# Optimization experiments

Measured on AMD Instinct MI355X. Metric: run time of the kernel, lower is better.

## Reference

```python
import jax, jax.numpy as jnp
import numpy as np

N_GRAMS = 3
N_KERNELS = 11

def _kernel_mus(K):
    l = [1.0]
    if K == 1:
        return l
    bs = 2.0 / (K - 1)
    l.append(1.0 - bs / 2.0)
    for i in range(1, K - 1):
        l.append(l[i] - bs)
    return l

def _kernel_sigmas(K):
    if K == 1:
        return [0.001]
    bs = 2.0 / (K - 1)
    return [0.001] + [0.5 * bs] * (K - 1)

MU = jnp.asarray(_kernel_mus(N_KERNELS), jnp.float32)       # (K,)
SIGMA = jnp.asarray(_kernel_sigmas(N_KERNELS), jnp.float32)  # (K,)

def _conv_relu(x, w, b):
    # x: (B,E,L), w: (O,E,h); right-pad h-1 so output length == L (as ConstantPad1d((0,h-1)))
    h = w.shape[-1]
    y = jax.lax.conv_general_dilated(x, w, (1,), [(0, h - 1)], dimension_numbers=('NCH', 'OIH', 'NCH'))
    return jax.nn.relu(y + b[None, :, None]).transpose(0, 2, 1)  # (B,L,O)

def _cosine(a, b):
    # CosineMatrixAttention: normalize rows then matmul
    an = a / (jnp.linalg.norm(a, axis=-1, keepdims=True) + 1e-13)
    bn = b / (jnp.linalg.norm(b, axis=-1, keepdims=True) + 1e-13)
    return jnp.einsum('bqe,bde->bqd', an, bn)

def setup_inputs() -> dict:
    key = jax.random.key(0)
    ks = jax.random.split(key, 12)
    B, Lq, Ld, V, E, O = 128, 64, 512, 30000, 300, 128
    inp = {}
    inp['tokens_q'] = jax.random.randint(ks[0], (B, Lq), 0, V)
    inp['tokens_d'] = jax.random.randint(ks[1], (B, Ld), 0, V)
    inp['emb'] = jax.random.normal(ks[2], (V, E), jnp.float32) * 0.1
    for i, h in enumerate((1, 2, 3)):
        inp['conv_w%d' % h] = jax.random.normal(ks[3 + i], (O, E, h), jnp.float32) * (1.0 / np.sqrt(E * h))
        inp['conv_b%d' % h] = jnp.zeros((O,), jnp.float32)
    inp['fc_w'] = jax.random.normal(ks[9], (1, N_KERNELS * N_GRAMS * N_GRAMS), jnp.float32) * 0.1
    inp['fc_b'] = jnp.zeros((1,), jnp.float32)
    return inp

def reference(tokens_q, tokens_d, emb, conv_w1, conv_b1, conv_w2, conv_b2, conv_w3, conv_b3, fc_w, fc_b):
    qmask = (tokens_q > 0).astype(jnp.float32)  # (B,Lq)
    dmask = (tokens_d > 0).astype(jnp.float32)  # (B,Ld)
    qe = emb[tokens_q].transpose(0, 2, 1)  # (B,E,Lq)
    de = emb[tokens_d].transpose(0, 2, 1)  # (B,E,Ld)
    cws = [(conv_w1, conv_b1), (conv_w2, conv_b2), (conv_w3, conv_b3)]
    hq = [_conv_relu(qe, w, b) for w, b in cws]  # each (B,Lq,O)
    hd = [_conv_relu(de, w, b) for w, b in cws]  # each (B,Ld,O)
    pair_mask = qmask[:, :, None] * dmask[:, None, :]  # (B,Lq,Ld)
    mu = MU[None, None, None, :]
    sig = SIGMA[None, None, None, :]
    feats = []
    for q in range(N_GRAMS):
        for d in range(N_GRAMS):
            m = _cosine(hq[q], hd[d]) * pair_mask  # (B,Lq,Ld)
            rbf = jnp.exp(-jnp.square(m[..., None] - mu) / (2.0 * jnp.square(sig))) * pair_mask[..., None]
            qk = rbf.sum(axis=2)  # (B,Lq,K)
            logk = jnp.log(jnp.maximum(qk, 1e-10)) * 0.01
            # NOTE: original has a typo (loq_ vs log_) so the query mask is NOT applied before summing
            feats.append(logk.sum(axis=1))  # (B,K)
    cross = jnp.concatenate(feats, axis=-1)  # (B, K*G*G)
    return cross @ fc_w.T + fc_b  # (B,1)
```

## Files before the change

kernel.cpp:

```cpp
#include <hip/hip_runtime.h>
#include <hip/hip_bf16.h>

typedef __attribute__((ext_vector_type(8))) short short8;
typedef __attribute__((ext_vector_type(4))) float f32x4;
typedef __attribute__((ext_vector_type(2))) unsigned int u32x2;

#define E_DIM 300
#define NCH   128
#define NOUT  384
#define NCHUNK 30

#define OPITCH 792

#define GLD16(gp, lp) __builtin_amdgcn_global_load_lds( \
    (const __attribute__((address_space(1))) unsigned int*)(const void*)(gp), \
    (__attribute__((address_space(3))) unsigned int*)(void*)(lp), 16, 0, 0)

__device__ __forceinline__ unsigned short f2bf(float f) {
    unsigned int u = __float_as_uint(f);
    u += 0x7FFFu + ((u >> 16) & 1u);
    return (unsigned short)(u >> 16);
}

__device__ __forceinline__ void xcd_map(int bx, int& b, int& p) {
    int x = bx & 7;
    int j = bx >> 3;
    b = x * 16 + j / 9;
    p = j - (j / 9) * 9;
}

__global__ void pack_wb(const float* __restrict__ w1, const float* __restrict__ w2,
                        const float* __restrict__ w3, unsigned short* __restrict__ Wp) {
    int idx = blockIdx.x * 256 + threadIdx.x;
    if (idx >= NCHUNK * NOUT * 32) return;
    int ke = idx & 31;
    int n  = (idx >> 5) % NOUT;
    int c  = idx / (32 * NOUT);
    int s  = c / 10;
    int e  = (c % 10) * 32 + ke;
    int g  = n >> 7, o = n & 127, h = g + 1;
    float v = 0.0f;
    if (e < E_DIM && s < h) {
        const float* w = (g == 0) ? w1 : ((g == 1) ? w2 : w3);
        v = w[(o * E_DIM + e) * h + s];
    }
    Wp[idx] = f2bf(v);
}

__global__ void pack_emb(const float* __restrict__ emb, unsigned short* __restrict__ embh) {
    int u = blockIdx.x * 256 + threadIdx.x;
    if (u >= 30000 * 40) return;
    int row = u / 40;
    int c8  = u - row * 40;
    int col = c8 * 8;
    ushort4 lo = {0, 0, 0, 0}, hi = {0, 0, 0, 0};
    const float* src = emb + (size_t)row * E_DIM + col;
    if (col + 8 <= E_DIM) {
        float4 a = *(const float4*)src;
        float4 c = *(const float4*)(src + 4);
        lo.x = f2bf(a.x); lo.y = f2bf(a.y); lo.z = f2bf(a.z); lo.w = f2bf(a.w);
        hi.x = f2bf(c.x); hi.y = f2bf(c.y); hi.z = f2bf(c.z); hi.w = f2bf(c.w);
    } else if (col < E_DIM) {
        float4 a = *(const float4*)src;
        lo.x = f2bf(a.x); lo.y = f2bf(a.y); lo.z = f2bf(a.z); lo.w = f2bf(a.w);
    }
    unsigned short* dst = embh + (size_t)row * 320 + col;
    *(ushort4*)dst       = lo;
    *(ushort4*)(dst + 4) = hi;
}

__launch_bounds__(512, 4)
__global__ void conv_mfma(const int* __restrict__ tokens_q, const int* __restrict__ tokens_d,
                          const unsigned short* __restrict__ embh, const unsigned short* __restrict__ Wp,
                          const float* __restrict__ b1, const float* __restrict__ b2,
                          const float* __restrict__ b3,
                          unsigned short* __restrict__ hq, unsigned short* __restrict__ hd) {
    __shared__ __align__(16) char lds[64 * OPITCH];
    __shared__ float nrm[64 * 3];

    int b, tile;
    xcd_map(blockIdx.x, b, tile);
    int isq  = (tile == 0);
    int L    = isq ? 64 : 512;
    int t0   = isq ? 0 : (tile - 1) * 64;
    const int* toks = isq ? (tokens_q + b * 64) : (tokens_d + b * 512);
    int tid  = threadIdx.x;
    int lane = tid & 63;
    int wn   = tid >> 6;
    int lr   = lane & 15;
    int lg   = lane >> 4;

    if (tid < 192) nrm[tid] = 0.0f;

    const unsigned short* __restrict__ wpB = Wp + (size_t)(wn * 16 + lr) * 32 + lg * 8;
    short8 bb[2][3];
    #pragma unroll
    for (int g = 0; g < 3; ++g) {
        bb[0][g] = *(const short8*)(wpB + (size_t)(0 * NOUT + g * 128) * 32);
        bb[1][g] = *(const short8*)(wpB + (size_t)(1 * NOUT + g * 128) * 32);
    }

    {
        auto gather_row = [&](int r, int sl) {
            int pos = t0 + r;
            int tk  = (pos < L) ? toks[pos] : -1;
            char* wbase = lds + r * 640;
            int xr = (r & 7) << 4;
            if (tk >= 0) {
                const unsigned short* src = embh + (size_t)tk * 320 + sl * 8;
                uint4 v[5];
                #pragma unroll
                for (int k = 0; k < 5; ++k) v[k] = *(const uint4*)(src + k * 64);
                #pragma unroll
                for (int k = 0; k < 5; ++k)
                    *(uint4*)(wbase + (((sl + 8 * k) * 16) ^ xr)) = v[k];
            } else {
                uint4 z = {0, 0, 0, 0};
                #pragma unroll
                for (int k = 0; k < 5; ++k)
                    *(uint4*)(wbase + (((sl + 8 * k) * 16) ^ xr)) = z;
            }
        };
        gather_row(tid >> 3, tid & 7);
        if (tid < 16) gather_row(64 + (tid >> 3), tid & 7);
    }
    __syncthreads();

    f32x4 acc[4][3];
    #pragma unroll
    for (int i = 0; i < 4; ++i)
        #pragma unroll
        for (int g = 0; g < 3; ++g) acc[i][g] = (f32x4){0.f, 0.f, 0.f, 0.f};

    #pragma unroll
    for (int c = 0; c < NCHUNK; ++c) {
        const int S  = (c >= 20) ? 2 : ((c >= 10) ? 1 : 0);
        const int ec = c - S * 10;
        short8 a[4];
        #pragma unroll
        for (int i = 0; i < 4; ++i) {
            int row = i * 16 + lr + S;
            int byt = (ec * 64 + lg * 16) ^ ((row & 7) << 4);
            a[i] = *(const short8*)(lds + row * 640 + byt);
        }
        #pragma unroll
        for (int i = 0; i < 4; ++i)
            #pragma unroll
            for (int g = S; g < 3; ++g)
                acc[i][g] = __builtin_amdgcn_mfma_f32_16x16x32_bf16(a[i], bb[c & 1][g], acc[i][g], 0, 0, 0);
        if (c < NCHUNK - 2) {
            const int S2 = ((c + 2) >= 20) ? 2 : (((c + 2) >= 10) ? 1 : 0);
            #pragma unroll
            for (int g = S2; g < 3; ++g)
                bb[c & 1][g] = *(const short8*)(wpB + (size_t)((c + 2) * NOUT + g * 128) * 32);
        }
    }

    #pragma unroll
    for (int g = 0; g < 3; ++g) {
        float bv = (g == 0 ? b1 : (g == 1 ? b2 : b3))[wn * 16 + lr];
        #pragma unroll
        for (int i = 0; i < 4; ++i)
            #pragma unroll
            for (int r = 0; r < 4; ++r) {
                float v = acc[i][g][r] + bv;
                v = v > 0.0f ? v : 0.0f;
                acc[i][g][r] = v;
                float s = v * v;
                s += __shfl_xor(s, 1, 16);
                s += __shfl_xor(s, 2, 16);
                s += __shfl_xor(s, 4, 16);
                s += __shfl_xor(s, 8, 16);
                if (lr == 0) atomicAdd(&nrm[(i * 16 + lg * 4 + r) * 3 + g], s);
            }
    }
    __syncthreads();

    if (tid < 192) nrm[tid] = 1.0f / (sqrtf(nrm[tid]) + 1e-13f);
    __syncthreads();

    unsigned short* os = (unsigned short*)lds;
    #pragma unroll
    for (int i = 0; i < 4; ++i)
        #pragma unroll
        for (int r = 0; r < 4; ++r) {
            int row = i * 16 + lg * 4 + r;
            #pragma unroll
            for (int g = 0; g < 3; ++g)
                os[row * (OPITCH / 2) + g * 128 + wn * 16 + lr] = f2bf(acc[i][g][r] * nrm[row * 3 + g]);
        }
    __syncthreads();

    unsigned short* outp = isq ? hq : hd;
    #pragma unroll
    for (int it = 0; it < 12; ++it) {
        int idx = it * 512 + tid;
        int row = idx / 96;
        int c8  = idx - row * 96;
        int g   = c8 >> 5;
        int ch  = (c8 & 31) * 4;
        u32x2 v = *(const u32x2*)(lds + row * OPITCH + c8 * 8);
        __builtin_nontemporal_store(v, (u32x2*)&outp[((size_t)(g * 128 + b) * L + t0 + row) * NCH + ch]);
    }
}

__launch_bounds__(256, 2)
__global__ void sim_rbf(const unsigned short* __restrict__ hq,
                        const unsigned short* __restrict__ hd,
                        const int* __restrict__ tokens_q, const int* __restrict__ tokens_d,
                        float* __restrict__ cross) {
    __shared__ __align__(16) short ds2[2][64 * 128];
    __shared__ unsigned char dm_s[512];
    __shared__ float logk_s[11];

    int b, p;
    xcd_map(blockIdx.x, b, p);
    int gq = p / 3;
    int gd = p % 3;
    int tid = threadIdx.x;
    int lane = tid & 63;
    int wn   = tid >> 6;
    int lr   = lane & 15;
    int lg   = lane >> 4;

    if (tid < 11) logk_s[tid] = 0.0f;

    const unsigned short* qsrc = hq + ((size_t)(gq * 128 + b) * 64) * NCH;
    const unsigned short* dsrc = hd + ((size_t)(gd * 128 + b) * 512) * NCH;

    int q  = wn * 16 + lr;
    float qm = (tokens_q[b * 64 + q] > 0) ? 1.0f : 0.0f;

    int rloc = 4 * wn + (lane >> 4);
    int cu   = (lane & 15) ^ (rloc & 7);

    auto stage = [&](int bufI, int ch) {
        const unsigned short* s0 = dsrc + ((size_t)ch * 64 + rloc) * NCH + cu * 8;
        #pragma unroll
        for (int it = 0; it < 4; ++it)
            GLD16(s0 + (size_t)it * 16 * NCH, &ds2[bufI][(it * 16 + 4 * wn) * 128]);
    };

    stage(0, 0);
    for (int i = tid; i < 512; i += 256)
        dm_s[i] = (tokens_d[b * 512 + i] > 0) ? 1 : 0;
    __syncthreads();

    float qk[11];
    #pragma unroll
    for (int k = 0; k < 11; ++k) qk[k] = 0.0f;

    const float C4 = 0.0183156389f;

    for (int ch = 0; ch < 8; ++ch) {
        int buf = ch & 1;
        if (ch < 7) stage(buf ^ 1, ch + 1);

        short8 qf[4];
        #pragma unroll
        for (int ks = 0; ks < 4; ++ks)
            qf[ks] = *(const short8*)&qsrc[q * NCH + ks * 32 + lg * 8];

        #pragma unroll
        for (int mt = 0; mt < 4; ++mt) {
            int r = mt * 16 + lr;
            f32x4 acc = (f32x4){0.f, 0.f, 0.f, 0.f};
            #pragma unroll
            for (int ks = 0; ks < 4; ++ks) {
                short8 a = *(const short8*)((const char*)&ds2[buf][0]
                              + r * 256 + (((ks * 4 + lg) ^ (r & 7)) << 4));
                acc = __builtin_amdgcn_mfma_f32_16x16x32_bf16(a, qf[ks], acc, 0, 0, 0);
            }
            uchar4 du = *(const uchar4*)&dm_s[ch * 64 + mt * 16 + lg * 4];
            float cv[4], cm[4];
            cm[0] = qm * (float)du.x; cm[1] = qm * (float)du.y;
            cm[2] = qm * (float)du.z; cm[3] = qm * (float)du.w;
            #pragma unroll
            for (int r2 = 0; r2 < 4; ++r2) cv[r2] = acc[r2] * cm[r2];

            float cmx = fmaxf(fmaxf(cv[0], cv[1]), fmaxf(cv[2], cv[3]));
            if (__any(cmx > 0.98f)) {
                #pragma unroll
                for (int r2 = 0; r2 < 4; ++r2) {
                    if (cv[r2] > 0.98f) {
                        float t0 = cv[r2] - 1.0f;
                        qk[0] += __expf(-500000.0f * t0 * t0);
                    }
                }
            }
            #pragma unroll
            for (int r2 = 0; r2 < 4; ++r2) {
                float c  = cv[r2];
                float tA = c - 0.1f;
                float TA = __expf(-50.0f * tA * tA) * cm[r2];
                float UA = __expf(20.0f * c - 4.0f);
                float s  = C4 * __builtin_amdgcn_rcpf(UA);
                float TB = TA * s;
                float UB = C4 * s;
                qk[5] += TA;
                TA *= UA; qk[4] += TA; UA *= C4;
                TA *= UA; qk[3] += TA; UA *= C4;
                TA *= UA; qk[2] += TA; UA *= C4;
                TA *= UA; qk[1] += TA;
                qk[6] += TB;
                TB *= UB; qk[7] += TB; UB *= C4;
                TB *= UB; qk[8] += TB; UB *= C4;
                TB *= UB; qk[9] += TB; UB *= C4;
                TB *= UB; qk[10] += TB;
            }
        }

        __syncthreads();
    }

    #pragma unroll
    for (int k = 0; k < 11; ++k) {
        float v = qk[k];
        v += __shfl_xor(v, 16);
        v += __shfl_xor(v, 32);
        qk[k] = v;
    }
    if (lg == 0) {
        #pragma unroll
        for (int k = 0; k < 11; ++k) {
            float lv = __logf(fmaxf(qk[k], 1e-10f)) * 0.01f;
            atomicAdd(&logk_s[k], lv);
        }
    }
    __syncthreads();
    if (tid < 11) cross[b * 99 + p * 11 + tid] = logk_s[tid];
}

__global__ void fc_kernel(const float* __restrict__ cross, const float* __restrict__ fc_w,
                          const float* __restrict__ fc_b, float* __restrict__ out) {
    int b = threadIdx.x;
    float acc = fc_b[0];
    #pragma unroll 11
    for (int j = 0; j < 99; ++j) acc += cross[b * 99 + j] * fc_w[j];
    out[b] = acc;
}

extern "C" void kernel_launch(void* const* d_in, const int* in_sizes, int n_in,
                              void* d_out, int out_size, void* d_ws, size_t ws_size,
                              hipStream_t stream) {
    const int*   tq  = (const int*)d_in[0];
    const int*   td  = (const int*)d_in[1];
    const float* emb = (const float*)d_in[2];
    const float* w1  = (const float*)d_in[3];
    const float* cb1 = (const float*)d_in[4];
    const float* w2  = (const float*)d_in[5];
    const float* cb2 = (const float*)d_in[6];
    const float* w3  = (const float*)d_in[7];
    const float* cb3 = (const float*)d_in[8];
    const float* fcw = (const float*)d_in[9];
    const float* fcb = (const float*)d_in[10];

    char* ws = (char*)d_ws;
    unsigned short* Wp    = (unsigned short*)ws;
    float*          cross = (float*)(ws + 921600);
    unsigned short* hq    = (unsigned short*)(ws + 1048576);
    unsigned short* hd    = (unsigned short*)(ws + 8388608);
    unsigned short* embh  = (unsigned short*)(ws + 58720256);

    hipLaunchKernelGGL(pack_wb, dim3(1440), dim3(256), 0, stream, w1, w2, w3, Wp);
    hipLaunchKernelGGL(pack_emb, dim3(4688), dim3(256), 0, stream, emb, embh);
    hipLaunchKernelGGL(conv_mfma, dim3(128 * 9), dim3(512), 0, stream,
                       tq, td, embh, Wp, cb1, cb2, cb3, hq, hd);
    hipLaunchKernelGGL(sim_rbf, dim3(128 * 9), dim3(256), 0, stream, hq, hd, tq, td, cross);
    hipLaunchKernelGGL(fc_kernel, dim3(1), dim3(128), 0, stream, cross, fcw, fcb, (float*)d_out);
}
```

Baseline: 171.3 us.

## Merge pack kernels and read doc tiles directly from global in sim_rbf

```diff
diff --git a/kernel.cpp b/kernel.cpp
--- a/kernel.cpp
+++ b/kernel.cpp
@@ -11,10 +11,6 @@
 #define NCHUNK 30
 
 #define OPITCH 792
-
-#define GLD16(gp, lp) __builtin_amdgcn_global_load_lds( \
-    (const __attribute__((address_space(1))) unsigned int*)(const void*)(gp), \
-    (__attribute__((address_space(3))) unsigned int*)(void*)(lp), 16, 0, 0)
 
 __device__ __forceinline__ unsigned short f2bf(float f) {
     unsigned int u = __float_as_uint(f);
@@ -29,44 +25,46 @@
     p = j - (j / 9) * 9;
 }
 
-__global__ void pack_wb(const float* __restrict__ w1, const float* __restrict__ w2,
-                        const float* __restrict__ w3, unsigned short* __restrict__ Wp) {
-    int idx = blockIdx.x * 256 + threadIdx.x;
-    if (idx >= NCHUNK * NOUT * 32) return;
-    int ke = idx & 31;
-    int n  = (idx >> 5) % NOUT;
-    int c  = idx / (32 * NOUT);
-    int s  = c / 10;
-    int e  = (c % 10) * 32 + ke;
-    int g  = n >> 7, o = n & 127, h = g + 1;
-    float v = 0.0f;
-    if (e < E_DIM && s < h) {
-        const float* w = (g == 0) ? w1 : ((g == 1) ? w2 : w3);
-        v = w[(o * E_DIM + e) * h + s];
-    }
-    Wp[idx] = f2bf(v);
-}
-
-__global__ void pack_emb(const float* __restrict__ emb, unsigned short* __restrict__ embh) {
-    int u = blockIdx.x * 256 + threadIdx.x;
-    if (u >= 30000 * 40) return;
-    int row = u / 40;
-    int c8  = u - row * 40;
-    int col = c8 * 8;
-    ushort4 lo = {0, 0, 0, 0}, hi = {0, 0, 0, 0};
-    const float* src = emb + (size_t)row * E_DIM + col;
-    if (col + 8 <= E_DIM) {
-        float4 a = *(const float4*)src;
-        float4 c = *(const float4*)(src + 4);
-        lo.x = f2bf(a.x); lo.y = f2bf(a.y); lo.z = f2bf(a.z); lo.w = f2bf(a.w);
-        hi.x = f2bf(c.x); hi.y = f2bf(c.y); hi.z = f2bf(c.z); hi.w = f2bf(c.w);
-    } else if (col < E_DIM) {
-        float4 a = *(const float4*)src;
-        lo.x = f2bf(a.x); lo.y = f2bf(a.y); lo.z = f2bf(a.z); lo.w = f2bf(a.w);
-    }
-    unsigned short* dst = embh + (size_t)row * 320 + col;
-    *(ushort4*)dst       = lo;
-    *(ushort4*)(dst + 4) = hi;
+__global__ void pack_all(const float* __restrict__ w1, const float* __restrict__ w2,
+                         const float* __restrict__ w3, const float* __restrict__ emb,
+                         unsigned short* __restrict__ Wp, unsigned short* __restrict__ embh) {
+    int bx = blockIdx.x;
+    if (bx < 1440) {
+        int idx = bx * 256 + threadIdx.x;
+        if (idx >= NCHUNK * NOUT * 32) return;
+        int ke = idx & 31;
+        int n  = (idx >> 5) % NOUT;
+        int c  = idx / (32 * NOUT);
+        int s  = c / 10;
+        int e  = (c % 10) * 32 + ke;
+        int g  = n >> 7, o = n & 127, h = g + 1;
+        float v = 0.0f;
+        if (e < E_DIM && s < h) {
+            const float* w = (g == 0) ? w1 : ((g == 1) ? w2 : w3);
+            v = w[(o * E_DIM + e) * h + s];
+        }
+        Wp[idx] = f2bf(v);
+    } else {
+        int u = (bx - 1440) * 256 + threadIdx.x;
+        if (u >= 30000 * 40) return;
+        int row = u / 40;
+        int c8  = u - row * 40;
+        int col = c8 * 8;
+        ushort4 lo = {0, 0, 0, 0}, hi = {0, 0, 0, 0};
+        const float* src = emb + (size_t)row * E_DIM + col;
+        if (col + 8 <= E_DIM) {
+            float4 a = *(const float4*)src;
+            float4 c = *(const float4*)(src + 4);
+            lo.x = f2bf(a.x); lo.y = f2bf(a.y); lo.z = f2bf(a.z); lo.w = f2bf(a.w);
+            hi.x = f2bf(c.x); hi.y = f2bf(c.y); hi.z = f2bf(c.z); hi.w = f2bf(c.w);
+        } else if (col < E_DIM) {
+            float4 a = *(const float4*)src;
+            lo.x = f2bf(a.x); lo.y = f2bf(a.y); lo.z = f2bf(a.z); lo.w = f2bf(a.w);
+        }
+        unsigned short* dst = embh + (size_t)row * 320 + col;
+        *(ushort4*)dst       = lo;
+        *(ushort4*)(dst + 4) = hi;
+    }
 }
 
 __launch_bounds__(512, 4)
@@ -209,7 +207,6 @@
                         const unsigned short* __restrict__ hd,
                         const int* __restrict__ tokens_q, const int* __restrict__ tokens_d,
                         float* __restrict__ cross) {
-    __shared__ __align__(16) short ds2[2][64 * 128];
     __shared__ unsigned char dm_s[512];
     __shared__ float logk_s[11];
 
@@ -224,6 +221,8 @@
     int lg   = lane >> 4;
 
     if (tid < 11) logk_s[tid] = 0.0f;
+    for (int i = tid; i < 512; i += 256)
+        dm_s[i] = (tokens_d[b * 512 + i] > 0) ? 1 : 0;
 
     const unsigned short* qsrc = hq + ((size_t)(gq * 128 + b) * 64) * NCH;
     const unsigned short* dsrc = hd + ((size_t)(gd * 128 + b) * 512) * NCH;
@@ -231,19 +230,11 @@
     int q  = wn * 16 + lr;
     float qm = (tokens_q[b * 64 + q] > 0) ? 1.0f : 0.0f;
 
-    int rloc = 4 * wn + (lane >> 4);
-    int cu   = (lane & 15) ^ (rloc & 7);
-
-    auto stage = [&](int bufI, int ch) {
-        const unsigned short* s0 = dsrc + ((size_t)ch * 64 + rloc) * NCH + cu * 8;
-        #pragma unroll
-        for (int it = 0; it < 4; ++it)
-            GLD16(s0 + (size_t)it * 16 * NCH, &ds2[bufI][(it * 16 + 4 * wn) * 128]);
-    };
-
-    stage(0, 0);
-    for (int i = tid; i < 512; i += 256)
-        dm_s[i] = (tokens_d[b * 512 + i] > 0) ? 1 : 0;
+    short8 qf[4];
+    #pragma unroll
+    for (int ks = 0; ks < 4; ++ks)
+        qf[ks] = *(const short8*)&qsrc[q * NCH + ks * 32 + lg * 8];
+
     __syncthreads();
 
     float qk[11];
@@ -253,22 +244,13 @@
     const float C4 = 0.0183156389f;
 
     for (int ch = 0; ch < 8; ++ch) {
-        int buf = ch & 1;
-        if (ch < 7) stage(buf ^ 1, ch + 1);
-
-        short8 qf[4];
-        #pragma unroll
-        for (int ks = 0; ks < 4; ++ks)
-            qf[ks] = *(const short8*)&qsrc[q * NCH + ks * 32 + lg * 8];
-
         #pragma unroll
         for (int mt = 0; mt < 4; ++mt) {
-            int r = mt * 16 + lr;
+            const unsigned short* dr = dsrc + ((size_t)(ch * 64 + mt * 16 + lr)) * NCH + lg * 8;
             f32x4 acc = (f32x4){0.f, 0.f, 0.f, 0.f};
             #pragma unroll
             for (int ks = 0; ks < 4; ++ks) {
-                short8 a = *(const short8*)((const char*)&ds2[buf][0]
-                              + r * 256 + (((ks * 4 + lg) ^ (r & 7)) << 4));
+                short8 a = *(const short8*)(dr + ks * 32);
                 acc = __builtin_amdgcn_mfma_f32_16x16x32_bf16(a, qf[ks], acc, 0, 0, 0);
             }
             uchar4 du = *(const uchar4*)&dm_s[ch * 64 + mt * 16 + lg * 4];
@@ -309,8 +291,6 @@
                 TB *= UB; qk[10] += TB;
             }
         }
-
-        __syncthreads();
     }
 
     #pragma unroll
@@ -362,8 +342,7 @@
     unsigned short* hd    = (unsigned short*)(ws + 8388608);
     unsigned short* embh  = (unsigned short*)(ws + 58720256);
 
-    hipLaunchKernelGGL(pack_wb, dim3(1440), dim3(256), 0, stream, w1, w2, w3, Wp);
-    hipLaunchKernelGGL(pack_emb, dim3(4688), dim3(256), 0, stream, emb, embh);
+    hipLaunchKernelGGL(pack_all, dim3(6128), dim3(256), 0, stream, w1, w2, w3, emb, Wp, embh);
     hipLaunchKernelGGL(conv_mfma, dim3(128 * 9), dim3(512), 0, stream,
                        tq, td, embh, Wp, cb1, cb2, cb3, hq, hd);
     hipLaunchKernelGGL(sim_rbf, dim3(128 * 9), dim3(256), 0, stream, hq, hd, tq, td, cross);
```

Result: slower. 179.8 us (+5.0%).
